# Kernel optimization log

Hardware: AMD Instinct MI355X
Metric: run time of the kernel (lower is better)

## Reference

```python
import jax, jax.numpy as jnp
import numpy as np

D_MODEL = 1024
N_HEADS = 16
HEAD_DIM = D_MODEL // N_HEADS


def setup_inputs() -> dict:
    key = jax.random.key(0)
    ks = jax.random.split(key, 5)
    B, T = 4, 2048
    scale = 0.02
    x = jax.random.normal(ks[0], (B, T, D_MODEL), dtype=jnp.float32)
    W_qkv = jax.random.normal(ks[1], (D_MODEL, 3 * D_MODEL), dtype=jnp.float32) * scale
    b_qkv = jnp.zeros((3 * D_MODEL,), dtype=jnp.float32)
    W_out = jax.random.normal(ks[2], (D_MODEL, D_MODEL), dtype=jnp.float32) * scale
    b_out = jnp.zeros((D_MODEL,), dtype=jnp.float32)
    return {"x": x, "W_qkv": W_qkv, "b_qkv": b_qkv, "W_out": W_out, "b_out": b_out}


def reference(x, W_qkv, b_qkv, W_out, b_out):
    B, T, C = x.shape
    H, Dh = N_HEADS, HEAD_DIM
    qkv = x @ W_qkv + b_qkv                      # (B,T,3C)
    q, k, v = jnp.split(qkv, 3, axis=-1)
    # (B,T,C) -> (B,H,T,Dh)
    q = q.reshape(B, T, H, Dh).transpose(0, 2, 1, 3)
    k = k.reshape(B, T, H, Dh).transpose(0, 2, 1, 3)
    v = v.reshape(B, T, H, Dh).transpose(0, 2, 1, 3)
    scores = jnp.einsum("bhqd,bhkd->bhqk", q, k) / jnp.sqrt(jnp.float32(Dh))
    causal = jnp.tril(jnp.ones((T, T), dtype=bool))  # True = keep
    scores = jnp.where(causal, scores, jnp.float32(-jnp.inf))
    attn = jax.nn.softmax(scores, axis=-1)
    out = jnp.einsum("bhqk,bhkd->bhqd", attn, v)  # (B,H,T,Dh)
    concat = out.transpose(0, 2, 1, 3).reshape(B, T, C)
    return concat @ W_out + b_out
```

## Files before the change

### kernel.cpp

```cpp
#include <hip/hip_runtime.h>
#include <math.h>

typedef __attribute__((ext_vector_type(8))) short bf16x8;
typedef __attribute__((ext_vector_type(4))) float f32x4;
typedef unsigned short u16;
typedef unsigned int u32;

#define TSEQ 2048
#define NH   16
#define DH   64
#define CDIM 1024

__device__ __forceinline__ u16 f2bf(float f) {
    union { float f; u32 u; } v; v.f = f;
    u32 r = v.u + 0x7fffu + ((v.u >> 16) & 1u);
    return (u16)(r >> 16);
}

__device__ __forceinline__ void gl_lds16(const void* g, void* l) {
    __builtin_amdgcn_global_load_lds(
        (const __attribute__((address_space(1))) u32*)g,
        (__attribute__((address_space(3))) u32*)l, 16, 0, 0);
}

#define MFMA16(a, b, c) __builtin_amdgcn_mfma_f32_16x16x32_bf16(a, b, c, 0, 0, 0)

__global__ __launch_bounds__(256) void cvt_bf16(const float* __restrict__ in,
                                                u16* __restrict__ out, int n) {
    int i = (blockIdx.x * 256 + threadIdx.x) * 8;
    if (i >= n) return;
    float4 a = *(const float4*)(in + i);
    float4 b = *(const float4*)(in + i + 4);
    u16 o[8] = {f2bf(a.x), f2bf(a.y), f2bf(a.z), f2bf(a.w),
                f2bf(b.x), f2bf(b.y), f2bf(b.z), f2bf(b.w)};
    *(uint4*)(out + i) = *(const uint4*)o;
}

__global__ __launch_bounds__(256) void tr_w_bf16(const float* __restrict__ Wf,
                                                 u16* __restrict__ Wt, int K, int N) {
    __shared__ float tile[32][33];
    int n0 = blockIdx.x * 32, k0 = blockIdx.y * 32;
    int tx = threadIdx.x, ty = threadIdx.y;
#pragma unroll
    for (int r = 0; r < 4; r++)
        tile[ty + r * 8][tx] = Wf[(k0 + ty + r * 8) * N + n0 + tx];
    __syncthreads();
#pragma unroll
    for (int r = 0; r < 4; r++)
        Wt[(n0 + ty + r * 8) * K + k0 + tx] = f2bf(tile[tx][ty + r * 8]);
}

__global__ __launch_bounds__(256) void tr_v_bf16(const u16* __restrict__ V,
                                                 u16* __restrict__ Vt) {
    __shared__ u16 Vl[64][72];
    const int tt = blockIdx.x, bh = blockIdx.y;
    const u16* src = V + (bh * TSEQ + tt * 64) * DH;
    const int tid = threadIdx.x;
#pragma unroll
    for (int r = 0; r < 2; r++) {
        int idx = r * 256 + tid;
        int row = idx >> 3, h = idx & 7;
        uint4 d4 = *(const uint4*)(src + row * DH + h * 8);
        *(uint4*)(&Vl[row][h * 8]) = d4;
    }
    __syncthreads();
    u16* dstb = Vt + bh * DH * TSEQ + tt * 64;
#pragma unroll
    for (int r = 0; r < 2; r++) {
        int idx = r * 256 + tid;
        int d = idx >> 3, ht = idx & 7;
        u16 o[8];
#pragma unroll
        for (int e = 0; e < 8; e++) o[e] = Vl[ht * 8 + e][d];
        *(uint4*)(dstb + d * TSEQ + ht * 8) = *(const uint4*)o;
    }
}

__global__ __launch_bounds__(256) void qkv_gemm_bf(
    const u16* __restrict__ A, const u16* __restrict__ Bt,
    const float* __restrict__ bias,
    u16* __restrict__ Qo, u16* __restrict__ Ko, u16* __restrict__ Vo) {
    __shared__ u16 Al[128 * 32];
    __shared__ u16 Bl[128 * 32];
    const int tid = threadIdx.x;
    const int lane = tid & 63, w = tid >> 6;
    const int l15 = lane & 15, l4 = lane >> 4;
    const int wm = w >> 1, wn = w & 1;
    const int mb = blockIdx.y * 128, nb = blockIdx.x * 128;
    const int KD = 1024;

    f32x4 zero = {0.f, 0.f, 0.f, 0.f};
    f32x4 acc[4][4];
#pragma unroll
    for (int i = 0; i < 4; i++)
#pragma unroll
        for (int j = 0; j < 4; j++) acc[i][j] = zero;

    for (int kb = 0; kb < KD; kb += 32) {
        __syncthreads();
#pragma unroll
        for (int r = 0; r < 2; r++) {
            int idx = r * 256 + tid;
            int row = idx >> 2, h = idx & 3;
            gl_lds16(A + (mb + row) * KD + kb + h * 8, Al + idx * 8);
            gl_lds16(Bt + (nb + row) * KD + kb + h * 8, Bl + idx * 8);
        }
        __syncthreads();
        bf16x8 af[4], bfr[4];
#pragma unroll
        for (int u = 0; u < 4; u++) {
            af[u]  = *(const bf16x8*)(Al + (wm * 64 + u * 16 + l15) * 32 + l4 * 8);
            bfr[u] = *(const bf16x8*)(Bl + (wn * 64 + u * 16 + l15) * 32 + l4 * 8);
        }
#pragma unroll
        for (int am = 0; am < 4; am++)
#pragma unroll
            for (int bn = 0; bn < 4; bn++)
                acc[am][bn] = MFMA16(af[am], bfr[bn], acc[am][bn]);
    }

#pragma unroll
    for (int am = 0; am < 4; am++)
#pragma unroll
        for (int bn = 0; bn < 4; bn++) {
            int n = nb + wn * 64 + bn * 16 + l15;
            int which = n >> 10, hh = (n >> 6) & 15, d = n & 63;
            u16* dst = (which == 0) ? Qo : ((which == 1) ? Ko : Vo);
            float bz = bias[n];
#pragma unroll
            for (int i = 0; i < 4; i++) {
                int m = mb + wm * 64 + am * 16 + l4 * 4 + i;
                int b = m >> 11, t = m & 2047;
                dst[((b * NH + hh) * TSEQ + t) * DH + d] = f2bf(acc[am][bn][i] + bz);
            }
        }
}

__global__ __launch_bounds__(256) void out_gemm_bf(
    const u16* __restrict__ A, const u16* __restrict__ Bt,
    const float* __restrict__ bias, float* __restrict__ Out) {
    __shared__ u16 Al[128 * 32];
    __shared__ u16 Bl[128 * 32];
    const int tid = threadIdx.x;
    const int lane = tid & 63, w = tid >> 6;
    const int l15 = lane & 15, l4 = lane >> 4;
    const int wm = w >> 1, wn = w & 1;
    const int mb = blockIdx.y * 128, nb = blockIdx.x * 128;
    const int KD = 1024;

    f32x4 zero = {0.f, 0.f, 0.f, 0.f};
    f32x4 acc[4][4];
#pragma unroll
    for (int i = 0; i < 4; i++)
#pragma unroll
        for (int j = 0; j < 4; j++) acc[i][j] = zero;

    for (int kb = 0; kb < KD; kb += 32) {
        __syncthreads();
#pragma unroll
        for (int r = 0; r < 2; r++) {
            int idx = r * 256 + tid;
            int row = idx >> 2, h = idx & 3;
            gl_lds16(A + (mb + row) * KD + kb + h * 8, Al + idx * 8);
            gl_lds16(Bt + (nb + row) * KD + kb + h * 8, Bl + idx * 8);
        }
        __syncthreads();
        bf16x8 af[4], bfr[4];
#pragma unroll
        for (int u = 0; u < 4; u++) {
            af[u]  = *(const bf16x8*)(Al + (wm * 64 + u * 16 + l15) * 32 + l4 * 8);
            bfr[u] = *(const bf16x8*)(Bl + (wn * 64 + u * 16 + l15) * 32 + l4 * 8);
        }
#pragma unroll
        for (int am = 0; am < 4; am++)
#pragma unroll
            for (int bn = 0; bn < 4; bn++)
                acc[am][bn] = MFMA16(af[am], bfr[bn], acc[am][bn]);
    }

#pragma unroll
    for (int am = 0; am < 4; am++)
#pragma unroll
        for (int bn = 0; bn < 4; bn++) {
            int n = nb + wn * 64 + bn * 16 + l15;
            float bz = bias[n];
#pragma unroll
            for (int i = 0; i < 4; i++) {
                int m = mb + wm * 64 + am * 16 + l4 * 4 + i;
                Out[m * CDIM + n] = acc[am][bn][i] + bz;
            }
        }
}

__global__ __launch_bounds__(256, 4) void attn_mfma(
    const u16* __restrict__ Q, const u16* __restrict__ K,
    const u16* __restrict__ Vt, u16* __restrict__ Oc) {
    __shared__ u16 Kl[2][4096];
    __shared__ u16 Vl[2][4096];
    __shared__ u16 Pl[4096];

    const int tid = threadIdx.x;
    const int lane = tid & 63, w = tid >> 6;
    const int l15 = lane & 15, l4 = lane >> 4;
    const int bh = blockIdx.x & 63;
    const int pair = blockIdx.x >> 6;
    const int qt0 = pair, qt1 = 31 - pair;
    const int nt0 = qt0 + 1;
    const int ntt = 33;

    const u16* Qb = Q + bh * TSEQ * DH;
    const u16* Kb = K + bh * TSEQ * DH;
    const u16* Vb = Vt + bh * DH * TSEQ;

    const int srow = tid >> 3;
    const float SCL = 0.18033688011112042f;

    auto STAGE = [&](int kt, int p) {
#pragma unroll
        for (int r = 0; r < 2; r++) {
            int idx = r * 256 + tid;
            int row = idx >> 3, h = idx & 7;
            int hs = h ^ (row & 7);
            gl_lds16(Kb + (kt * 64 + row) * DH + hs * 8, &Kl[p][idx * 8]);
            gl_lds16(Vb + row * TSEQ + kt * 64 + hs * 8, &Vl[p][idx * 8]);
        }
    };

    STAGE(0, 0);

    int sg = 0;
    const int b = bh >> 4, hh = bh & 15;

    for (int half = 0; half < 2; half++) {
        const int qt = half ? qt1 : qt0;
        const int q_row = qt * 64 + w * 16 + l15;

        bf16x8 qf0, qf1;
        {
            const u16* qp = Qb + q_row * DH + l4 * 8;
            qf0 = *(const bf16x8*)(qp);
            qf1 = *(const bf16x8*)(qp + 32);
        }

        f32x4 zero = {0.f, 0.f, 0.f, 0.f};
        f32x4 oacc[4];
        float m_r = -INFINITY, l_r = 0.f;
#pragma unroll
        for (int i = 0; i < 4; i++) oacc[i] = zero;

        for (int kt = 0; kt <= qt; kt++, sg++) {
            const int p = sg & 1;
            __syncthreads();
            int ns = sg + 1;
            if (ns < ntt) {
                int nkt = (ns < nt0) ? ns : (ns - nt0);
                STAGE(nkt, p ^ 1);
                asm volatile("s_waitcnt vmcnt(4)" ::: "memory");
            } else {
                asm volatile("s_waitcnt vmcnt(0)" ::: "memory");
            }
            __syncthreads();

            __builtin_amdgcn_s_setprio(1);
            f32x4 sacc[4];
#pragma unroll
            for (int c = 0; c < 4; c++) {
                int trow = c * 16 + l15;
                int sw = l15 & 7;
                bf16x8 kf0 = *(const bf16x8*)(&Kl[p][trow * 64 + (l4 ^ sw) * 8]);
                bf16x8 kf1 = *(const bf16x8*)(&Kl[p][trow * 64 + ((4 + l4) ^ sw) * 8]);
                f32x4 a = zero;
                a = MFMA16(kf0, qf0, a);
                a = MFMA16(kf1, qf1, a);
                sacc[c] = a;
            }
            __builtin_amdgcn_s_setprio(0);

            if (kt == qt) {
#pragma unroll
                for (int c = 0; c < 4; c++)
#pragma unroll
                    for (int i = 0; i < 4; i++) {
                        int kg = kt * 64 + c * 16 + l4 * 4 + i;
                        if (kg > q_row) sacc[c][i] = -INFINITY;
                    }
            }

            float mx = sacc[0][0];
#pragma unroll
            for (int c = 0; c < 4; c++)
#pragma unroll
                for (int i = 0; i < 4; i++) mx = fmaxf(mx, sacc[c][i]);
            mx = fmaxf(mx, __shfl_xor(mx, 16));
            mx = fmaxf(mx, __shfl_xor(mx, 32));
            float mnew = fmaxf(m_r, mx);
            float corr = __builtin_amdgcn_exp2f((m_r - mnew) * SCL);

            float pv[16];
            float rs = 0.f;
#pragma unroll
            for (int c = 0; c < 4; c++)
#pragma unroll
                for (int i = 0; i < 4; i++) {
                    float e = __builtin_amdgcn_exp2f((sacc[c][i] - mnew) * SCL);
                    pv[c * 4 + i] = e;
                    rs += e;
                }
            rs += __shfl_xor(rs, 16);
            rs += __shfl_xor(rs, 32);
            l_r = l_r * corr + rs;
            m_r = mnew;

#pragma unroll
            for (int c = 0; c < 4; c++) {
                u16 po[4];
#pragma unroll
                for (int i = 0; i < 4; i++) po[i] = f2bf(pv[c * 4 + i]);
                int g = (c << 1) + (l4 >> 1);
                int gp = g ^ (l15 & 7);
                *(uint2*)&Pl[w * 1024 + l15 * 64 + gp * 8 + ((l4 & 1) << 2)] =
                    *(const uint2*)po;
            }

            float cr[4];
#pragma unroll
            for (int r = 0; r < 4; r++) cr[r] = __shfl(corr, l4 * 4 + r);
#pragma unroll
            for (int dg = 0; dg < 4; dg++)
#pragma unroll
                for (int r = 0; r < 4; r++) oacc[dg][r] *= cr[r];

            __builtin_amdgcn_s_setprio(1);
#pragma unroll
            for (int kk = 0; kk < 2; kk++) {
                int grp = ((kk << 2) + l4) ^ (l15 & 7);
                bf16x8 pf = *(const bf16x8*)&Pl[w * 1024 + l15 * 64 + grp * 8];
#pragma unroll
                for (int dg = 0; dg < 4; dg++) {
                    int drow = (dg << 4) + l15;
                    bf16x8 vf = *(const bf16x8*)(&Vl[p][drow * 64 + grp * 8]);
                    oacc[dg] = MFMA16(pf, vf, oacc[dg]);
                }
            }
            __builtin_amdgcn_s_setprio(0);
        }

        float inv[4];
#pragma unroll
        for (int r = 0; r < 4; r++) inv[r] = 1.0f / __shfl(l_r, l4 * 4 + r);
        int tbase = qt * 64 + w * 16 + l4 * 4;
#pragma unroll
        for (int r = 0; r < 4; r++) {
            int t = tbase + r;
#pragma unroll
            for (int dg = 0; dg < 4; dg++)
                Oc[(b * TSEQ + t) * CDIM + hh * DH + (dg << 4) + l15] =
                    f2bf(oacc[dg][r] * inv[r]);
        }
    }
}

extern "C" void kernel_launch(void* const* d_in, const int* in_sizes, int n_in,
                              void* d_out, int out_size, void* d_ws, size_t ws_size,
                              hipStream_t stream) {
    const float* x     = (const float*)d_in[0];
    const float* W_qkv = (const float*)d_in[1];
    const float* b_qkv = (const float*)d_in[2];
    const float* W_out = (const float*)d_in[3];
    const float* b_out = (const float*)d_in[4];
    float* out = (float*)d_out;

    u16* xb  = (u16*)d_ws;
    u16* Wqt = xb  + 8388608;
    u16* Wot = Wqt + 3145728;
    u16* Qw  = Wot + 1048576;
    u16* Kw  = Qw  + 8388608;
    u16* Vw  = Kw  + 8388608;
    u16* Vtw = Vw  + 8388608;
    u16* Ocw = Vtw + 8388608;

    cvt_bf16<<<4096, 256, 0, stream>>>(x, xb, 8388608);
    tr_w_bf16<<<dim3(96, 32), dim3(32, 8), 0, stream>>>(W_qkv, Wqt, 1024, 3072);
    tr_w_bf16<<<dim3(32, 32), dim3(32, 8), 0, stream>>>(W_out, Wot, 1024, 1024);
    qkv_gemm_bf<<<dim3(24, 64), 256, 0, stream>>>(xb, Wqt, b_qkv, Qw, Kw, Vw);
    tr_v_bf16<<<dim3(32, 64), 256, 0, stream>>>(Vw, Vtw);
    attn_mfma<<<1024, 256, 0, stream>>>(Qw, Kw, Vtw, Ocw);
    out_gemm_bf<<<dim3(8, 64), 256, 0, stream>>>(Ocw, Wot, b_out, out);
}
```

Measured before the change: 273.7 us.

## Fuse V transpose into QKV epilogue and process paired query tiles jointly

```diff
diff --git a/kernel.cpp b/kernel.cpp
--- a/kernel.cpp
+++ b/kernel.cpp
@@ -10,11 +10,22 @@
 #define NH   16
 #define DH   64
 #define CDIM 1024
+#define SCLQ 0.18033688011112042f
 
 __device__ __forceinline__ u16 f2bf(float f) {
     union { float f; u32 u; } v; v.f = f;
     u32 r = v.u + 0x7fffu + ((v.u >> 16) & 1u);
     return (u16)(r >> 16);
+}
+
+__device__ __forceinline__ u32 cvtpk(float lo, float hi) {
+    u32 r;
+    asm("v_cvt_pk_bf16_f32 %0, %1, %2" : "=v"(r) : "v"(lo), "v"(hi));
+    return r;
+}
+
+__device__ __forceinline__ float max3f(float a, float b, float c) {
+    return fmaxf(fmaxf(a, b), c);
 }
 
 __device__ __forceinline__ void gl_lds16(const void* g, void* l) {
@@ -48,32 +59,6 @@
 #pragma unroll
     for (int r = 0; r < 4; r++)
         Wt[(n0 + ty + r * 8) * K + k0 + tx] = f2bf(tile[tx][ty + r * 8]);
-}
-
-__global__ __launch_bounds__(256) void tr_v_bf16(const u16* __restrict__ V,
-                                                 u16* __restrict__ Vt) {
-    __shared__ u16 Vl[64][72];
-    const int tt = blockIdx.x, bh = blockIdx.y;
-    const u16* src = V + (bh * TSEQ + tt * 64) * DH;
-    const int tid = threadIdx.x;
-#pragma unroll
-    for (int r = 0; r < 2; r++) {
-        int idx = r * 256 + tid;
-        int row = idx >> 3, h = idx & 7;
-        uint4 d4 = *(const uint4*)(src + row * DH + h * 8);
-        *(uint4*)(&Vl[row][h * 8]) = d4;
-    }
-    __syncthreads();
-    u16* dstb = Vt + bh * DH * TSEQ + tt * 64;
-#pragma unroll
-    for (int r = 0; r < 2; r++) {
-        int idx = r * 256 + tid;
-        int d = idx >> 3, ht = idx & 7;
-        u16 o[8];
-#pragma unroll
-        for (int e = 0; e < 8; e++) o[e] = Vl[ht * 8 + e][d];
-        *(uint4*)(dstb + d * TSEQ + ht * 8) = *(const uint4*)o;
-    }
 }
 
 __global__ __launch_bounds__(256) void qkv_gemm_bf(
@@ -125,13 +110,25 @@
         for (int bn = 0; bn < 4; bn++) {
             int n = nb + wn * 64 + bn * 16 + l15;
             int which = n >> 10, hh = (n >> 6) & 15, d = n & 63;
-            u16* dst = (which == 0) ? Qo : ((which == 1) ? Ko : Vo);
             float bz = bias[n];
-#pragma unroll
-            for (int i = 0; i < 4; i++) {
-                int m = mb + wm * 64 + am * 16 + l4 * 4 + i;
-                int b = m >> 11, t = m & 2047;
-                dst[((b * NH + hh) * TSEQ + t) * DH + d] = f2bf(acc[am][bn][i] + bz);
+            int m0 = mb + wm * 64 + am * 16 + l4 * 4;
+            int b = m0 >> 11, t0 = m0 & 2047;
+            if (which == 0) {
+#pragma unroll
+                for (int i = 0; i < 4; i++)
+                    Qo[((b * NH + hh) * TSEQ + t0 + i) * DH + d] =
+                        f2bf((acc[am][bn][i] + bz) * SCLQ);
+            } else if (which == 1) {
+#pragma unroll
+                for (int i = 0; i < 4; i++)
+                    Ko[((b * NH + hh) * TSEQ + t0 + i) * DH + d] =
+                        f2bf(acc[am][bn][i] + bz);
+            } else {
+                u16 ov[4];
+#pragma unroll
+                for (int i = 0; i < 4; i++) ov[i] = f2bf(acc[am][bn][i] + bz);
+                *(uint2*)&Vo[((b * NH + hh) * DH + d) * TSEQ + t0] =
+                    *(const uint2*)ov;
             }
         }
 }
@@ -205,15 +202,11 @@
     const int bh = blockIdx.x & 63;
     const int pair = blockIdx.x >> 6;
     const int qt0 = pair, qt1 = 31 - pair;
-    const int nt0 = qt0 + 1;
-    const int ntt = 33;
+    const int NT = qt1 + 1;
 
     const u16* Qb = Q + bh * TSEQ * DH;
     const u16* Kb = K + bh * TSEQ * DH;
     const u16* Vb = Vt + bh * DH * TSEQ;
-
-    const int srow = tid >> 3;
-    const float SCL = 0.18033688011112042f;
 
     auto STAGE = [&](int kt, int p) {
 #pragma unroll
@@ -226,137 +219,165 @@
         }
     };
 
+    const int qrow0 = qt0 * 64 + w * 16 + l15;
+    const int qrow1 = qt1 * 64 + w * 16 + l15;
+    bf16x8 q0a, q0b, q1a, q1b;
+    {
+        const u16* qp = Qb + qrow0 * DH + l4 * 8;
+        q0a = *(const bf16x8*)(qp);
+        q0b = *(const bf16x8*)(qp + 32);
+    }
+    {
+        const u16* qp = Qb + qrow1 * DH + l4 * 8;
+        q1a = *(const bf16x8*)(qp);
+        q1b = *(const bf16x8*)(qp + 32);
+    }
+
+    f32x4 zero = {0.f, 0.f, 0.f, 0.f};
+    f32x4 o0[4], o1[4];
+    float m0 = -INFINITY, l0 = 0.f, m1 = -INFINITY, l1 = 0.f;
+#pragma unroll
+    for (int i = 0; i < 4; i++) { o0[i] = zero; o1[i] = zero; }
+
+    auto SMPV = [&](f32x4* s, float& m_r, float& l_r, f32x4* oacc,
+                    int q_row, bool domask, int kt, int p) {
+        if (domask) {
+#pragma unroll
+            for (int c = 0; c < 4; c++)
+#pragma unroll
+                for (int i = 0; i < 4; i++) {
+                    int kg = kt * 64 + c * 16 + l4 * 4 + i;
+                    if (kg > q_row) s[c][i] = -INFINITY;
+                }
+        }
+        float a0 = max3f(s[0][0], s[0][1], s[0][2]);
+        float a1 = max3f(s[0][3], s[1][0], s[1][1]);
+        float a2 = max3f(s[1][2], s[1][3], s[2][0]);
+        float a3 = max3f(s[2][1], s[2][2], s[2][3]);
+        float a4 = max3f(s[3][0], s[3][1], s[3][2]);
+        float mx = max3f(max3f(a0, a1, a2), fmaxf(a3, a4), s[3][3]);
+        mx = fmaxf(mx, __shfl_xor(mx, 16));
+        mx = fmaxf(mx, __shfl_xor(mx, 32));
+        if (!__all(mx <= m_r)) {
+            float mnew = fmaxf(m_r, mx);
+            float corr = __builtin_amdgcn_exp2f(m_r - mnew);
+            l_r *= corr;
+            float cr[4];
+#pragma unroll
+            for (int r = 0; r < 4; r++) cr[r] = __shfl(corr, l4 * 4 + r);
+#pragma unroll
+            for (int dg = 0; dg < 4; dg++)
+#pragma unroll
+                for (int r = 0; r < 4; r++) oacc[dg][r] *= cr[r];
+            m_r = mnew;
+        }
+        float pv[16];
+#pragma unroll
+        for (int c = 0; c < 4; c++)
+#pragma unroll
+            for (int i = 0; i < 4; i++)
+                pv[c * 4 + i] = __builtin_amdgcn_exp2f(s[c][i] - m_r);
+        float t0 = (pv[0] + pv[1]) + (pv[2] + pv[3]);
+        float t1 = (pv[4] + pv[5]) + (pv[6] + pv[7]);
+        float t2 = (pv[8] + pv[9]) + (pv[10] + pv[11]);
+        float t3 = (pv[12] + pv[13]) + (pv[14] + pv[15]);
+        float rs = (t0 + t1) + (t2 + t3);
+        rs += __shfl_xor(rs, 16);
+        rs += __shfl_xor(rs, 32);
+        l_r += rs;
+
+#pragma unroll
+        for (int c = 0; c < 4; c++) {
+            uint2 pr;
+            pr.x = cvtpk(pv[c * 4 + 0], pv[c * 4 + 1]);
+            pr.y = cvtpk(pv[c * 4 + 2], pv[c * 4 + 3]);
+            int g = (c << 1) + (l4 >> 1);
+            int gp = g ^ (l15 & 7);
+            *(uint2*)&Pl[w * 1024 + l15 * 64 + gp * 8 + ((l4 & 1) << 2)] = pr;
+        }
+
+        __builtin_amdgcn_s_setprio(1);
+#pragma unroll
+        for (int kk = 0; kk < 2; kk++) {
+            int grp = ((kk << 2) + l4) ^ (l15 & 7);
+            bf16x8 pf = *(const bf16x8*)&Pl[w * 1024 + l15 * 64 + grp * 8];
+#pragma unroll
+            for (int dg = 0; dg < 4; dg++) {
+                int drow = (dg << 4) + l15;
+                bf16x8 vf = *(const bf16x8*)(&Vl[p][drow * 64 + grp * 8]);
+                oacc[dg] = MFMA16(pf, vf, oacc[dg]);
+            }
+        }
+        __builtin_amdgcn_s_setprio(0);
+    };
+
     STAGE(0, 0);
 
-    int sg = 0;
+    for (int kt = 0; kt < NT; kt++) {
+        const int p = kt & 1;
+        __syncthreads();
+        if (kt + 1 < NT) {
+            STAGE(kt + 1, p ^ 1);
+            asm volatile("s_waitcnt vmcnt(4)" ::: "memory");
+        } else {
+            asm volatile("s_waitcnt vmcnt(0)" ::: "memory");
+        }
+        __syncthreads();
+
+        const bool act0 = (kt <= qt0);
+
+        f32x4 s1[4], s0[4];
+        __builtin_amdgcn_s_setprio(1);
+#pragma unroll
+        for (int c = 0; c < 4; c++) {
+            int trow = c * 16 + l15;
+            int sw = l15 & 7;
+            bf16x8 kf0 = *(const bf16x8*)(&Kl[p][trow * 64 + (l4 ^ sw) * 8]);
+            bf16x8 kf1 = *(const bf16x8*)(&Kl[p][trow * 64 + ((4 + l4) ^ sw) * 8]);
+            f32x4 a = zero;
+            a = MFMA16(kf0, q1a, a);
+            a = MFMA16(kf1, q1b, a);
+            s1[c] = a;
+            if (act0) {
+                f32x4 b = zero;
+                b = MFMA16(kf0, q0a, b);
+                b = MFMA16(kf1, q0b, b);
+                s0[c] = b;
+            }
+        }
+        __builtin_amdgcn_s_setprio(0);
+
+        SMPV(s1, m1, l1, o1, qrow1, kt == qt1, kt, p);
+        if (act0) {
+            asm volatile("s_waitcnt lgkmcnt(0)" ::: "memory");
+            SMPV(s0, m0, l0, o0, qrow0, kt == qt0, kt, p);
+        }
+    }
+
     const int b = bh >> 4, hh = bh & 15;
-
-    for (int half = 0; half < 2; half++) {
-        const int qt = half ? qt1 : qt0;
-        const int q_row = qt * 64 + w * 16 + l15;
-
-        bf16x8 qf0, qf1;
-        {
-            const u16* qp = Qb + q_row * DH + l4 * 8;
-            qf0 = *(const bf16x8*)(qp);
-            qf1 = *(const bf16x8*)(qp + 32);
-        }
-
-        f32x4 zero = {0.f, 0.f, 0.f, 0.f};
-        f32x4 oacc[4];
-        float m_r = -INFINITY, l_r = 0.f;
-#pragma unroll
-        for (int i = 0; i < 4; i++) oacc[i] = zero;
-
-        for (int kt = 0; kt <= qt; kt++, sg++) {
-            const int p = sg & 1;
-            __syncthreads();
-            int ns = sg + 1;
-            if (ns < ntt) {
-                int nkt = (ns < nt0) ? ns : (ns - nt0);
-                STAGE(nkt, p ^ 1);
-                asm volatile("s_waitcnt vmcnt(4)" ::: "memory");
-            } else {
-                asm volatile("s_waitcnt vmcnt(0)" ::: "memory");
-            }
-            __syncthreads();
-
-            __builtin_amdgcn_s_setprio(1);
-            f32x4 sacc[4];
-#pragma unroll
-            for (int c = 0; c < 4; c++) {
-                int trow = c * 16 + l15;
-                int sw = l15 & 7;
-                bf16x8 kf0 = *(const bf16x8*)(&Kl[p][trow * 64 + (l4 ^ sw) * 8]);
-                bf16x8 kf1 = *(const bf16x8*)(&Kl[p][trow * 64 + ((4 + l4) ^ sw) * 8]);
-                f32x4 a = zero;
-                a = MFMA16(kf0, qf0, a);
-                a = MFMA16(kf1, qf1, a);
-                sacc[c] = a;
-            }
-            __builtin_amdgcn_s_setprio(0);
-
-            if (kt == qt) {
-#pragma unroll
-                for (int c = 0; c < 4; c++)
-#pragma unroll
-                    for (int i = 0; i < 4; i++) {
-                        int kg = kt * 64 + c * 16 + l4 * 4 + i;
-                        if (kg > q_row) sacc[c][i] = -INFINITY;
-                    }
-            }
-
-            float mx = sacc[0][0];
-#pragma unroll
-            for (int c = 0; c < 4; c++)
-#pragma unroll
-                for (int i = 0; i < 4; i++) mx = fmaxf(mx, sacc[c][i]);
-            mx = fmaxf(mx, __shfl_xor(mx, 16));
-            mx = fmaxf(mx, __shfl_xor(mx, 32));
-            float mnew = fmaxf(m_r, mx);
-            float corr = __builtin_amdgcn_exp2f((m_r - mnew) * SCL);
-
-            float pv[16];
-            float rs = 0.f;
-#pragma unroll
-            for (int c = 0; c < 4; c++)
-#pragma unroll
-                for (int i = 0; i < 4; i++) {
-                    float e = __builtin_amdgcn_exp2f((sacc[c][i] - mnew) * SCL);
-                    pv[c * 4 + i] = e;
-                    rs += e;
-                }
-            rs += __shfl_xor(rs, 16);
-            rs += __shfl_xor(rs, 32);
-            l_r = l_r * corr + rs;
-            m_r = mnew;
-
-#pragma unroll
-            for (int c = 0; c < 4; c++) {
-                u16 po[4];
-#pragma unroll
-                for (int i = 0; i < 4; i++) po[i] = f2bf(pv[c * 4 + i]);
-                int g = (c << 1) + (l4 >> 1);
-                int gp = g ^ (l15 & 7);
-                *(uint2*)&Pl[w * 1024 + l15 * 64 + gp * 8 + ((l4 & 1) << 2)] =
-                    *(const uint2*)po;
-            }
-
-            float cr[4];
-#pragma unroll
-            for (int r = 0; r < 4; r++) cr[r] = __shfl(corr, l4 * 4 + r);
+    {
+        float inv[4];
+#pragma unroll
+        for (int r = 0; r < 4; r++) inv[r] = 1.0f / __shfl(l0, l4 * 4 + r);
+        int tb = qt0 * 64 + w * 16 + l4 * 4;
+#pragma unroll
+        for (int r = 0; r < 4; r++)
 #pragma unroll
             for (int dg = 0; dg < 4; dg++)
-#pragma unroll
-                for (int r = 0; r < 4; r++) oacc[dg][r] *= cr[r];
-
-            __builtin_amdgcn_s_setprio(1);
-#pragma unroll
-            for (int kk = 0; kk < 2; kk++) {
-                int grp = ((kk << 2) + l4) ^ (l15 & 7);
-                bf16x8 pf = *(const bf16x8*)&Pl[w * 1024 + l15 * 64 + grp * 8];
-#pragma unroll
-                for (int dg = 0; dg < 4; dg++) {
-                    int drow = (dg << 4) + l15;
-                    bf16x8 vf = *(const bf16x8*)(&Vl[p][drow * 64 + grp * 8]);
-                    oacc[dg] = MFMA16(pf, vf, oacc[dg]);
-                }
-            }
-            __builtin_amdgcn_s_setprio(0);
-        }
-
+                Oc[(b * TSEQ + tb + r) * CDIM + hh * DH + (dg << 4) + l15] =
+                    f2bf(o0[dg][r] * inv[r]);
+    }
+    {
         float inv[4];
 #pragma unroll
-        for (int r = 0; r < 4; r++) inv[r] = 1.0f / __shfl(l_r, l4 * 4 + r);
-        int tbase = qt * 64 + w * 16 + l4 * 4;
-#pragma unroll
-        for (int r = 0; r < 4; r++) {
-            int t = tbase + r;
+        for (int r = 0; r < 4; r++) inv[r] = 1.0f / __shfl(l1, l4 * 4 + r);
+        int tb = qt1 * 64 + w * 16 + l4 * 4;
+#pragma unroll
+        for (int r = 0; r < 4; r++)
 #pragma unroll
             for (int dg = 0; dg < 4; dg++)
-                Oc[(b * TSEQ + t) * CDIM + hh * DH + (dg << 4) + l15] =
-                    f2bf(oacc[dg][r] * inv[r]);
-        }
+                Oc[(b * TSEQ + tb + r) * CDIM + hh * DH + (dg << 4) + l15] =
+                    f2bf(o1[dg][r] * inv[r]);
     }
 }
 
@@ -375,15 +396,13 @@
     u16* Wot = Wqt + 3145728;
     u16* Qw  = Wot + 1048576;
     u16* Kw  = Qw  + 8388608;
-    u16* Vw  = Kw  + 8388608;
-    u16* Vtw = Vw  + 8388608;
+    u16* Vtw = Kw  + 8388608;
     u16* Ocw = Vtw + 8388608;
 
     cvt_bf16<<<4096, 256, 0, stream>>>(x, xb, 8388608);
     tr_w_bf16<<<dim3(96, 32), dim3(32, 8), 0, stream>>>(W_qkv, Wqt, 1024, 3072);
     tr_w_bf16<<<dim3(32, 32), dim3(32, 8), 0, stream>>>(W_out, Wot, 1024, 1024);
-    qkv_gemm_bf<<<dim3(24, 64), 256, 0, stream>>>(xb, Wqt, b_qkv, Qw, Kw, Vw);
-    tr_v_bf16<<<dim3(32, 64), 256, 0, stream>>>(Vw, Vtw);
+    qkv_gemm_bf<<<dim3(24, 64), 256, 0, stream>>>(xb, Wqt, b_qkv, Qw, Kw, Vtw);
     attn_mfma<<<1024, 256, 0, stream>>>(Qw, Kw, Vtw, Ocw);
     out_gemm_bf<<<dim3(8, 64), 256, 0, stream>>>(Ocw, Wot, b_out, out);
 }
```

New measurement: 271.9 us. Within noise of the previous version (-0.7%).
